# Kernel tuning notes

Hardware: AMD Instinct MI355X
Metric: run time of the kernel (lower is better)

## Reference

```python
import jax, jax.numpy as jnp
import numpy as np

N = 50000      # nodes
E = 800000     # edges (avg degree 16)
D_IN = 128
D_H = 128
D_OUT = 64


def setup_inputs() -> dict:
    key = jax.random.key(0)
    k_x, k_e, k_w1, k_b1, k_w2, k_b2 = jax.random.split(key, 6)
    x = jax.random.normal(k_x, (N, D_IN), dtype=jnp.float32)
    edge_index = jax.random.randint(k_e, (2, E), 0, N, dtype=jnp.int32)
    # Glorot-style init for GCN weights, zero bias (as in PyG GCNConv defaults)
    W1 = jax.random.normal(k_w1, (D_IN, D_H), dtype=jnp.float32) * (1.0 / np.sqrt(D_IN))
    b1 = jnp.zeros((D_H,), dtype=jnp.float32)
    W2 = jax.random.normal(k_w2, (D_H, D_OUT), dtype=jnp.float32) * (1.0 / np.sqrt(D_H))
    b2 = jnp.zeros((D_OUT,), dtype=jnp.float32)
    return {"x": x, "edge_index": edge_index, "W1": W1, "b1": b1, "W2": W2, "b2": b2}


def _gcn_norm(edge_index, n):
    # PyG gcn_norm with add_self_loops=True, edge_weight = 1
    loops = jnp.arange(n, dtype=edge_index.dtype)
    src = jnp.concatenate([edge_index[0], loops])  # [E+N]
    dst = jnp.concatenate([edge_index[1], loops])
    deg = jax.ops.segment_sum(jnp.ones_like(dst, dtype=jnp.float32), dst, num_segments=n)
    dinv = jnp.where(deg > 0, jax.lax.rsqrt(deg), 0.0)
    norm = dinv[src] * dinv[dst]                   # [E+N]
    return src, dst, norm


def _gcn_conv(h, src, dst, norm, W, b, n):
    # transform -> gather source -> scale by symmetric norm -> scatter-add at dst -> bias
    hW = h @ W                                      # [N, F_out]
    msg = hW[src] * norm[:, None]                   # [E+N, F_out]
    agg = jax.ops.segment_sum(msg, dst, num_segments=n)
    return agg + b


def reference(x, edge_index, W1, b1, W2, b2):
    n = x.shape[0]
    src, dst, norm = _gcn_norm(edge_index, n)
    x1 = jax.nn.relu(_gcn_conv(x, src, dst, norm, W1, b1, n))
    x2 = _gcn_conv(x1, src, dst, norm, W2, b2, n)
    return x2
```

## Files before the change

### kernel.cpp

```cpp
#include <hip/hip_runtime.h>

#define CAP  64
#define BN   64
#define NBMAX 1024
#define ECAP 2048
#define P1E  4096

typedef unsigned int uint;
typedef unsigned short ushort;
typedef __attribute__((ext_vector_type(8))) short short8;
typedef __attribute__((ext_vector_type(4))) float f32x4;

__device__ inline ushort f2bf(float f) {
    uint u = __float_as_uint(f);
    return (ushort)((u + 0x7fffu + ((u >> 16) & 1u)) >> 16);
}
__device__ inline uint packbf2(float lo, float hi) {
    return (uint)f2bf(lo) | ((uint)f2bf(hi) << 16);
}
__device__ inline void unpackbf2(uint u, float& lo, float& hi) {
    lo = __uint_as_float(u << 16);
    hi = __uint_as_float(u & 0xffff0000u);
}

__global__ __launch_bounds__(256) void k_init(const float* __restrict__ W1,
                                              const float* __restrict__ W2,
                                              ushort* __restrict__ W1t,
                                              ushort* __restrict__ W2t,
                                              int* __restrict__ gtail) {
    int i = blockIdx.x * 256 + threadIdx.x;
    if (i < NBMAX) gtail[i] = 0;
    if (i < 4 * 128 * 32) {
        int kt = i >> 12;
        int nn = (i >> 5) & 127;
        int ko = i & 31;
        W1t[i] = f2bf(W1[(size_t)(kt * 32 + ko) * 128 + nn]);
    }
    int j = i - 4 * 128 * 32;
    if (j >= 0 && j < 4 * 64 * 32) {
        int kt = j >> 11;
        int nn = (j >> 5) & 63;
        int ko = j & 31;
        W2t[j] = f2bf(W2[(size_t)(kt * 32 + ko) * 64 + nn]);
    }
}

__global__ __launch_bounds__(256) void k_part(const int* __restrict__ esrc,
                                              const int* __restrict__ edst,
                                              int E, int nb,
                                              int* __restrict__ gtail,
                                              uint* __restrict__ ebuf) {
    __shared__ int hist[NBMAX];
    int base_e = blockIdx.x * P1E;
    for (int i = threadIdx.x; i < nb; i += 256) hist[i] = 0;
    __syncthreads();

    int d[16], s[16];
#pragma unroll
    for (int u = 0; u < 16; u++) {
        int e = base_e + u * 256 + threadIdx.x;
        d[u] = (e < E) ? edst[e] : -1;
        s[u] = (e < E) ? esrc[e] : 0;
        if (d[u] >= 0) atomicAdd(&hist[d[u] >> 6], 1);
    }
    __syncthreads();

    for (int i = threadIdx.x; i < nb; i += 256) {
        int h = hist[i];
        hist[i] = (h > 0) ? atomicAdd(&gtail[i], h) : 0;
    }
    __syncthreads();

#pragma unroll
    for (int u = 0; u < 16; u++) {
        if (d[u] >= 0) {
            int b = d[u] >> 6;
            int slot = atomicAdd(&hist[b], 1);
            if (slot < ECAP)
                ebuf[(size_t)b * ECAP + slot] =
                    ((uint)(d[u] & (BN - 1)) << 16) | (uint)s[u];
        }
    }
}

__global__ __launch_bounds__(256) void k_csr(const uint* __restrict__ ebuf,
                                             const int* __restrict__ gtail,
                                             int n,
                                             ushort* __restrict__ colbuf,
                                             int* __restrict__ cnt,
                                             float* __restrict__ dinv) {
    __shared__ ushort cb[BN * CAP];
    __shared__ int cl[BN];
    int b = blockIdx.x;
    int ne = gtail[b];
    if (ne > ECAP) ne = ECAP;
    for (int i = threadIdx.x; i < BN; i += 256) cl[i] = 0;
    __syncthreads();

    const uint* eb = ebuf + (size_t)b * ECAP;
    for (int i = threadIdx.x; i < ne; i += 256) {
        uint pr = eb[i];
        int dloc = pr >> 16;
        int p = atomicAdd(&cl[dloc], 1);
        if (p < CAP) cb[dloc * CAP + p] = (ushort)(pr & 0xffffu);
    }
    __syncthreads();

    int node0 = b * BN;
    for (int i = threadIdx.x; i < BN * CAP / 8; i += 256) {
        int node = node0 + i / (CAP / 8);
        if (node < n)
            ((uint4*)&colbuf[(size_t)node0 * CAP])[i] = ((const uint4*)cb)[i];
    }
    for (int i = threadIdx.x; i < BN; i += 256) {
        int node = node0 + i;
        if (node < n) {
            int c = cl[i];
            dinv[node] = rsqrtf((float)c + 1.0f);
            cnt[node] = (c > CAP) ? CAP : c;
        }
    }
}

__global__ __launch_bounds__(256) void k_mgemm1(const float* __restrict__ Xf,
                                                const ushort* __restrict__ Wt,
                                                ushort* __restrict__ Yb, int n) {
    __shared__ ushort Ws[4 * 128 * 32];
    for (int idx = threadIdx.x; idx < 4 * 128 * 32 / 8; idx += 256)
        ((uint4*)Ws)[idx] = ((const uint4*)Wt)[idx];
    __syncthreads();

    int wid  = threadIdx.x >> 6;
    int l    = threadIdx.x & 63;
    int mrow = l & 15;
    int kgrp = l >> 4;
    int row16 = (blockIdx.x * 4 + wid) * 16;
    int r  = row16 + mrow;
    int rc = (r < n) ? r : (n - 1);

    f32x4 acc[8];
#pragma unroll
    for (int t = 0; t < 8; t++) acc[t] = (f32x4){0.f, 0.f, 0.f, 0.f};

#pragma unroll
    for (int kt = 0; kt < 4; kt++) {
        const float* xp = &Xf[(size_t)rc * 128 + kt * 32 + kgrp * 8];
        float4 x0 = *(const float4*)xp;
        float4 x1 = *(const float4*)(xp + 4);
        short8 a;
        a[0] = (short)f2bf(x0.x); a[1] = (short)f2bf(x0.y);
        a[2] = (short)f2bf(x0.z); a[3] = (short)f2bf(x0.w);
        a[4] = (short)f2bf(x1.x); a[5] = (short)f2bf(x1.y);
        a[6] = (short)f2bf(x1.z); a[7] = (short)f2bf(x1.w);
#pragma unroll
        for (int t = 0; t < 8; t++) {
            short8 b = *(const short8*)&Ws[((kt * 128) + t * 16 + mrow) * 32 + kgrp * 8];
            acc[t] = __builtin_amdgcn_mfma_f32_16x16x32_bf16(a, b, acc[t], 0, 0, 0);
        }
    }

    int orow = row16 + kgrp * 4;
#pragma unroll
    for (int t = 0; t < 8; t++) {
#pragma unroll
        for (int q = 0; q < 4; q++) {
            int rr = orow + q;
            if (rr < n) Yb[(size_t)rr * 128 + t * 16 + mrow] = f2bf(acc[t][q]);
        }
    }
}

__global__ __launch_bounds__(1024) void k_agg1m(const ushort* __restrict__ Hb,
                                                const int* __restrict__ cntc,
                                                const ushort* __restrict__ colbuf,
                                                const float* __restrict__ dinv,
                                                const float* __restrict__ b1,
                                                const ushort* __restrict__ W2t,
                                                ushort* __restrict__ Yb2, int n) {
    __shared__ ushort x1s[64 * 128];
    __shared__ ushort Ws[4 * 64 * 32];
    for (int idx = threadIdx.x; idx < 4 * 64 * 32 / 8; idx += 1024)
        ((uint4*)Ws)[idx] = ((const uint4*)W2t)[idx];

    const int CH = 128, LPG = 16;
    int grp  = threadIdx.x / LPG;
    int lane = threadIdx.x % LPG;
    int gid  = blockIdx.x * 64 + grp;
    int gc   = (gid < n) ? gid : (n - 1);

    float di = dinv[gc];
    int c = cntc[gc];
    if (c > CAP) c = CAP;

    float acc[8];
#pragma unroll
    for (int k = 0; k < 8; k++) acc[k] = 0.f;

    const ushort* cb = colbuf + (size_t)gc * CAP;
    for (int j = 0; j < c; j += 8) {
        uint4 iv = *(const uint4*)(cb + j);
        int s[8];
        s[0] = iv.x & 0xffff; s[1] = iv.x >> 16;
        s[2] = iv.y & 0xffff; s[3] = iv.y >> 16;
        s[4] = iv.z & 0xffff; s[5] = iv.z >> 16;
        s[6] = iv.w & 0xffff; s[7] = iv.w >> 16;
#pragma unroll
        for (int u = 1; u < 8; u++) if (j + u >= c) s[u] = s[0];
        float w[8];
#pragma unroll
        for (int u = 0; u < 8; u++)
            w[u] = (j + u < c) ? dinv[s[u]] : 0.f;
        uint4 h[8];
#pragma unroll
        for (int u = 0; u < 8; u++)
            h[u] = *(const uint4*)(Hb + (size_t)s[u] * CH + lane * 8);
#pragma unroll
        for (int u = 0; u < 8; u++) {
            float f0, f1;
            unpackbf2(h[u].x, f0, f1); acc[0] += f0 * w[u]; acc[1] += f1 * w[u];
            unpackbf2(h[u].y, f0, f1); acc[2] += f0 * w[u]; acc[3] += f1 * w[u];
            unpackbf2(h[u].z, f0, f1); acc[4] += f0 * w[u]; acc[5] += f1 * w[u];
            unpackbf2(h[u].w, f0, f1); acc[6] += f0 * w[u]; acc[7] += f1 * w[u];
        }
    }

    uint4 aself = *(const uint4*)(Hb + (size_t)gc * CH + lane * 8);
    float sf[8];
    unpackbf2(aself.x, sf[0], sf[1]);
    unpackbf2(aself.y, sf[2], sf[3]);
    unpackbf2(aself.z, sf[4], sf[5]);
    unpackbf2(aself.w, sf[6], sf[7]);

    float4 bb0 = *(const float4*)&b1[lane * 8];
    float4 bb1 = *(const float4*)&b1[lane * 8 + 4];
    float bb[8] = {bb0.x, bb0.y, bb0.z, bb0.w, bb1.x, bb1.y, bb1.z, bb1.w};

    float xv[8];
#pragma unroll
    for (int k = 0; k < 8; k++)
        xv[k] = fmaxf((acc[k] + di * sf[k]) * di + bb[k], 0.f);

    uint up[4] = { packbf2(xv[0], xv[1]), packbf2(xv[2], xv[3]),
                   packbf2(xv[4], xv[5]), packbf2(xv[6], xv[7]) };
    int slot = lane ^ (grp & 7);
    *(uint4*)&x1s[grp * 128 + slot * 8] = *(uint4*)up;

    __syncthreads();

    int wv = threadIdx.x >> 6;
    int l  = threadIdx.x & 63;
    int wr = wv >> 2, wc = wv & 3;
    int mrow = l & 15, kgrp = l >> 4;
    int arow = wr * 16 + mrow;

    f32x4 a2 = (f32x4){0.f, 0.f, 0.f, 0.f};
#pragma unroll
    for (int kt = 0; kt < 4; kt++) {
        int slotA = (kt * 4 + kgrp) ^ (arow & 7);
        short8 a = *(const short8*)&x1s[arow * 128 + slotA * 8];
        short8 b = *(const short8*)&Ws[((kt * 64) + wc * 16 + mrow) * 32 + kgrp * 8];
        a2 = __builtin_amdgcn_mfma_f32_16x16x32_bf16(a, b, a2, 0, 0, 0);
    }

    int row0 = blockIdx.x * 64 + wr * 16 + kgrp * 4;
#pragma unroll
    for (int q = 0; q < 4; q++) {
        int rr = row0 + q;
        if (rr < n) Yb2[(size_t)rr * 64 + wc * 16 + mrow] = f2bf(a2[q]);
    }
}

__global__ __launch_bounds__(256) void k_agg2(const ushort* __restrict__ Hb,
                                              const int* __restrict__ cntc,
                                              const ushort* __restrict__ colbuf,
                                              const float* __restrict__ dinv,
                                              const float* __restrict__ b2,
                                              float* __restrict__ out, int n) {
    const int CH = 64, LPG = 8;
    int t    = blockIdx.x * 256 + threadIdx.x;
    int gid  = t / LPG;
    int lane = t % LPG;
    if (gid >= n) return;

    float di = dinv[gid];
    int c = cntc[gid];
    if (c > CAP) c = CAP;

    float acc[8];
#pragma unroll
    for (int k = 0; k < 8; k++) acc[k] = 0.f;

    const ushort* cb = colbuf + (size_t)gid * CAP;
    for (int j = 0; j < c; j += 8) {
        uint4 iv = *(const uint4*)(cb + j);
        int s[8];
        s[0] = iv.x & 0xffff; s[1] = iv.x >> 16;
        s[2] = iv.y & 0xffff; s[3] = iv.y >> 16;
        s[4] = iv.z & 0xffff; s[5] = iv.z >> 16;
        s[6] = iv.w & 0xffff; s[7] = iv.w >> 16;
#pragma unroll
        for (int u = 1; u < 8; u++) if (j + u >= c) s[u] = s[0];
        float w[8];
#pragma unroll
        for (int u = 0; u < 8; u++)
            w[u] = (j + u < c) ? dinv[s[u]] : 0.f;
        uint4 h[8];
#pragma unroll
        for (int u = 0; u < 8; u++)
            h[u] = *(const uint4*)(Hb + (size_t)s[u] * CH + lane * 8);
#pragma unroll
        for (int u = 0; u < 8; u++) {
            float f0, f1;
            unpackbf2(h[u].x, f0, f1); acc[0] += f0 * w[u]; acc[1] += f1 * w[u];
            unpackbf2(h[u].y, f0, f1); acc[2] += f0 * w[u]; acc[3] += f1 * w[u];
            unpackbf2(h[u].z, f0, f1); acc[4] += f0 * w[u]; acc[5] += f1 * w[u];
            unpackbf2(h[u].w, f0, f1); acc[6] += f0 * w[u]; acc[7] += f1 * w[u];
        }
    }

    uint4 aself = *(const uint4*)(Hb + (size_t)gid * CH + lane * 8);
    float sf[8];
    unpackbf2(aself.x, sf[0], sf[1]);
    unpackbf2(aself.y, sf[2], sf[3]);
    unpackbf2(aself.z, sf[4], sf[5]);
    unpackbf2(aself.w, sf[6], sf[7]);

    float4 bb0 = *(const float4*)&b2[lane * 8];
    float4 bb1 = *(const float4*)&b2[lane * 8 + 4];
    float bb[8] = {bb0.x, bb0.y, bb0.z, bb0.w, bb1.x, bb1.y, bb1.z, bb1.w};

    float o[8];
#pragma unroll
    for (int k = 0; k < 8; k++)
        o[k] = (acc[k] + di * sf[k]) * di + bb[k];

    float* dst = out + (size_t)gid * CH + lane * 8;
    *(float4*)dst       = make_float4(o[0], o[1], o[2], o[3]);
    *(float4*)(dst + 4) = make_float4(o[4], o[5], o[6], o[7]);
}

extern "C" void kernel_launch(void* const* d_in, const int* in_sizes, int n_in,
                              void* d_out, int out_size, void* d_ws, size_t ws_size,
                              hipStream_t stream) {
    const float* x  = (const float*)d_in[0];
    const int*   ei = (const int*)d_in[1];
    const float* W1 = (const float*)d_in[2];
    const float* b1 = (const float*)d_in[3];
    const float* W2 = (const float*)d_in[4];
    const float* b2 = (const float*)d_in[5];
    float* out = (float*)d_out;

    int N = in_sizes[0] / 128;
    int E = in_sizes[1] / 2;
    const int* esrc = ei;
    const int* edst = ei + E;

    int nb = (N + BN - 1) / BN;

    char* ws = (char*)d_ws;
    size_t off = 0;
    auto alloc = [&](size_t bytes) -> void* {
        off = (off + 255) & ~(size_t)255;
        void* p = ws + off;
        off += bytes;
        return p;
    };
    int*    gtail   = (int*)   alloc((size_t)NBMAX * 4);
    int*    cnt     = (int*)   alloc((size_t)N * 4);
    float*  dinv    = (float*) alloc((size_t)N * 4);
    uint*   ebuf    = (uint*)  alloc((size_t)nb * ECAP * 4);
    ushort* colbuf  = (ushort*)alloc((size_t)nb * BN * CAP * 2 + 256);
    ushort* hW1b    = (ushort*)alloc((size_t)N * 128 * 2);
    ushort* hW2b    = (ushort*)alloc((size_t)N * 64 * 2);
    ushort* W1t     = (ushort*)alloc((size_t)4 * 128 * 32 * 2);
    ushort* W2t     = (ushort*)alloc((size_t)4 * 64 * 32 * 2);

    k_init<<<96, 256, 0, stream>>>(W1, W2, W1t, W2t, gtail);

    int nbP1 = (E + P1E - 1) / P1E;
    k_part<<<nbP1, 256, 0, stream>>>(esrc, edst, E, nb, gtail, ebuf);
    k_mgemm1<<<(N + 63) / 64, 256, 0, stream>>>(x, W1t, hW1b, N);
    k_csr<<<nb, 256, 0, stream>>>(ebuf, gtail, N, colbuf, cnt, dinv);

    k_agg1m<<<nb, 1024, 0, stream>>>(hW1b, cnt, colbuf, dinv, b1, W2t, hW2b, N);

    k_agg2<<<((size_t)N * 8 + 255) / 256, 256, 0, stream>>>(
        hW2b, cnt, colbuf, dinv, b2, out, N);
}
```

Measured before the change: 98.08 us.

## Split fused layer-1 aggregation and second GEMM into separate kernels

The fused 1024-thread aggregation+GEMM kernel is split into a 256-thread aggregation kernel that writes the layer-1 activations to a new bf16 buffer, plus a standalone MFMA GEMM kernel for the second layer. This removes the block-wide barrier and large shared-memory footprint so more blocks can be resident. Both aggregation kernels also gather 16 neighbors per iteration instead of 8 and hoist the self-row and bias loads ahead of the loop to expose more memory parallelism. The cost is an extra launch and a round-trip of the N×128 bf16 activations through global memory, plus higher register pressure from the wider unroll.

```diff
diff --git a/kernel.cpp b/kernel.cpp
--- a/kernel.cpp
+++ b/kernel.cpp
@@ -170,52 +170,94 @@
     }
 }
 
-__global__ __launch_bounds__(1024) void k_agg1m(const ushort* __restrict__ Hb,
-                                                const int* __restrict__ cntc,
-                                                const ushort* __restrict__ colbuf,
-                                                const float* __restrict__ dinv,
-                                                const float* __restrict__ b1,
-                                                const ushort* __restrict__ W2t,
-                                                ushort* __restrict__ Yb2, int n) {
-    __shared__ ushort x1s[64 * 128];
+__global__ __launch_bounds__(256) void k_mgemm2(const ushort* __restrict__ Xh,
+                                                const ushort* __restrict__ Wt,
+                                                ushort* __restrict__ Yb, int n) {
     __shared__ ushort Ws[4 * 64 * 32];
-    for (int idx = threadIdx.x; idx < 4 * 64 * 32 / 8; idx += 1024)
-        ((uint4*)Ws)[idx] = ((const uint4*)W2t)[idx];
-
+    for (int idx = threadIdx.x; idx < 4 * 64 * 32 / 8; idx += 256)
+        ((uint4*)Ws)[idx] = ((const uint4*)Wt)[idx];
+    __syncthreads();
+
+    int wid  = threadIdx.x >> 6;
+    int l    = threadIdx.x & 63;
+    int mrow = l & 15;
+    int kgrp = l >> 4;
+    int row16 = (blockIdx.x * 4 + wid) * 16;
+    int r  = row16 + mrow;
+    int rc = (r < n) ? r : (n - 1);
+
+    f32x4 acc[4];
+#pragma unroll
+    for (int t = 0; t < 4; t++) acc[t] = (f32x4){0.f, 0.f, 0.f, 0.f};
+
+#pragma unroll
+    for (int kt = 0; kt < 4; kt++) {
+        short8 a = *(const short8*)&Xh[(size_t)rc * 128 + kt * 32 + kgrp * 8];
+#pragma unroll
+        for (int t = 0; t < 4; t++) {
+            short8 b = *(const short8*)&Ws[((kt * 64) + t * 16 + mrow) * 32 + kgrp * 8];
+            acc[t] = __builtin_amdgcn_mfma_f32_16x16x32_bf16(a, b, acc[t], 0, 0, 0);
+        }
+    }
+
+    int orow = row16 + kgrp * 4;
+#pragma unroll
+    for (int t = 0; t < 4; t++) {
+#pragma unroll
+        for (int q = 0; q < 4; q++) {
+            int rr = orow + q;
+            if (rr < n) Yb[(size_t)rr * 64 + t * 16 + mrow] = f2bf(acc[t][q]);
+        }
+    }
+}
+
+__global__ __launch_bounds__(256) void k_agg1(const ushort* __restrict__ Hb,
+                                              const int* __restrict__ cntc,
+                                              const ushort* __restrict__ colbuf,
+                                              const float* __restrict__ dinv,
+                                              const float* __restrict__ b1,
+                                              ushort* __restrict__ x1b, int n) {
     const int CH = 128, LPG = 16;
-    int grp  = threadIdx.x / LPG;
-    int lane = threadIdx.x % LPG;
-    int gid  = blockIdx.x * 64 + grp;
-    int gc   = (gid < n) ? gid : (n - 1);
-
-    float di = dinv[gc];
-    int c = cntc[gc];
+    int t    = blockIdx.x * 256 + threadIdx.x;
+    int gid  = t / LPG;
+    int lane = t % LPG;
+    if (gid >= n) return;
+
+    float di = dinv[gid];
+    int c = cntc[gid];
     if (c > CAP) c = CAP;
 
+    uint4 aself = *(const uint4*)(Hb + (size_t)gid * CH + lane * 8);
+    float4 bb0 = *(const float4*)&b1[lane * 8];
+    float4 bb1 = *(const float4*)&b1[lane * 8 + 4];
+
     float acc[8];
 #pragma unroll
     for (int k = 0; k < 8; k++) acc[k] = 0.f;
 
-    const ushort* cb = colbuf + (size_t)gc * CAP;
-    for (int j = 0; j < c; j += 8) {
-        uint4 iv = *(const uint4*)(cb + j);
-        int s[8];
-        s[0] = iv.x & 0xffff; s[1] = iv.x >> 16;
-        s[2] = iv.y & 0xffff; s[3] = iv.y >> 16;
-        s[4] = iv.z & 0xffff; s[5] = iv.z >> 16;
-        s[6] = iv.w & 0xffff; s[7] = iv.w >> 16;
-#pragma unroll
-        for (int u = 1; u < 8; u++) if (j + u >= c) s[u] = s[0];
-        float w[8];
-#pragma unroll
-        for (int u = 0; u < 8; u++)
+    const ushort* cb = colbuf + (size_t)gid * CAP;
+    for (int j = 0; j < c; j += 16) {
+        uint4 iv0 = *(const uint4*)(cb + j);
+        uint4 iv1 = *(const uint4*)(cb + j + 8);
+        uint ivw[8] = {iv0.x, iv0.y, iv0.z, iv0.w, iv1.x, iv1.y, iv1.z, iv1.w};
+        int s[16];
+#pragma unroll
+        for (int u = 0; u < 8; u++) {
+            s[2 * u]     = ivw[u] & 0xffff;
+            s[2 * u + 1] = ivw[u] >> 16;
+        }
+#pragma unroll
+        for (int u = 1; u < 16; u++) if (j + u >= c) s[u] = s[0];
+        float w[16];
+#pragma unroll
+        for (int u = 0; u < 16; u++)
             w[u] = (j + u < c) ? dinv[s[u]] : 0.f;
-        uint4 h[8];
-#pragma unroll
-        for (int u = 0; u < 8; u++)
+        uint4 h[16];
+#pragma unroll
+        for (int u = 0; u < 16; u++)
             h[u] = *(const uint4*)(Hb + (size_t)s[u] * CH + lane * 8);
 #pragma unroll
-        for (int u = 0; u < 8; u++) {
+        for (int u = 0; u < 16; u++) {
             float f0, f1;
             unpackbf2(h[u].x, f0, f1); acc[0] += f0 * w[u]; acc[1] += f1 * w[u];
             unpackbf2(h[u].y, f0, f1); acc[2] += f0 * w[u]; acc[3] += f1 * w[u];
@@ -224,15 +266,11 @@
         }
     }
 
-    uint4 aself = *(const uint4*)(Hb + (size_t)gc * CH + lane * 8);
     float sf[8];
     unpackbf2(aself.x, sf[0], sf[1]);
     unpackbf2(aself.y, sf[2], sf[3]);
     unpackbf2(aself.z, sf[4], sf[5]);
     unpackbf2(aself.w, sf[6], sf[7]);
-
-    float4 bb0 = *(const float4*)&b1[lane * 8];
-    float4 bb1 = *(const float4*)&b1[lane * 8 + 4];
     float bb[8] = {bb0.x, bb0.y, bb0.z, bb0.w, bb1.x, bb1.y, bb1.z, bb1.w};
 
     float xv[8];
@@ -242,32 +280,7 @@
 
     uint up[4] = { packbf2(xv[0], xv[1]), packbf2(xv[2], xv[3]),
                    packbf2(xv[4], xv[5]), packbf2(xv[6], xv[7]) };
-    int slot = lane ^ (grp & 7);
-    *(uint4*)&x1s[grp * 128 + slot * 8] = *(uint4*)up;
-
-    __syncthreads();
-
-    int wv = threadIdx.x >> 6;
-    int l  = threadIdx.x & 63;
-    int wr = wv >> 2, wc = wv & 3;
-    int mrow = l & 15, kgrp = l >> 4;
-    int arow = wr * 16 + mrow;
-
-    f32x4 a2 = (f32x4){0.f, 0.f, 0.f, 0.f};
-#pragma unroll
-    for (int kt = 0; kt < 4; kt++) {
-        int slotA = (kt * 4 + kgrp) ^ (arow & 7);
-        short8 a = *(const short8*)&x1s[arow * 128 + slotA * 8];
-        short8 b = *(const short8*)&Ws[((kt * 64) + wc * 16 + mrow) * 32 + kgrp * 8];
-        a2 = __builtin_amdgcn_mfma_f32_16x16x32_bf16(a, b, a2, 0, 0, 0);
-    }
-
-    int row0 = blockIdx.x * 64 + wr * 16 + kgrp * 4;
-#pragma unroll
-    for (int q = 0; q < 4; q++) {
-        int rr = row0 + q;
-        if (rr < n) Yb2[(size_t)rr * 64 + wc * 16 + mrow] = f2bf(a2[q]);
-    }
+    *(uint4*)&x1b[(size_t)gid * CH + lane * 8] = *(uint4*)up;
 }
 
 __global__ __launch_bounds__(256) void k_agg2(const ushort* __restrict__ Hb,
@@ -286,30 +299,37 @@
     int c = cntc[gid];
     if (c > CAP) c = CAP;
 
+    uint4 aself = *(const uint4*)(Hb + (size_t)gid * CH + lane * 8);
+    float4 bb0 = *(const float4*)&b2[lane * 8];
+    float4 bb1 = *(const float4*)&b2[lane * 8 + 4];
+
     float acc[8];
 #pragma unroll
     for (int k = 0; k < 8; k++) acc[k] = 0.f;
 
     const ushort* cb = colbuf + (size_t)gid * CAP;
-    for (int j = 0; j < c; j += 8) {
-        uint4 iv = *(const uint4*)(cb + j);
-        int s[8];
-        s[0] = iv.x & 0xffff; s[1] = iv.x >> 16;
-        s[2] = iv.y & 0xffff; s[3] = iv.y >> 16;
-        s[4] = iv.z & 0xffff; s[5] = iv.z >> 16;
-        s[6] = iv.w & 0xffff; s[7] = iv.w >> 16;
-#pragma unroll
-        for (int u = 1; u < 8; u++) if (j + u >= c) s[u] = s[0];
-        float w[8];
-#pragma unroll
-        for (int u = 0; u < 8; u++)
+    for (int j = 0; j < c; j += 16) {
+        uint4 iv0 = *(const uint4*)(cb + j);
+        uint4 iv1 = *(const uint4*)(cb + j + 8);
+        uint ivw[8] = {iv0.x, iv0.y, iv0.z, iv0.w, iv1.x, iv1.y, iv1.z, iv1.w};
+        int s[16];
+#pragma unroll
+        for (int u = 0; u < 8; u++) {
+            s[2 * u]     = ivw[u] & 0xffff;
+            s[2 * u + 1] = ivw[u] >> 16;
+        }
+#pragma unroll
+        for (int u = 1; u < 16; u++) if (j + u >= c) s[u] = s[0];
+        float w[16];
+#pragma unroll
+        for (int u = 0; u < 16; u++)
             w[u] = (j + u < c) ? dinv[s[u]] : 0.f;
-        uint4 h[8];
-#pragma unroll
-        for (int u = 0; u < 8; u++)
+        uint4 h[16];
+#pragma unroll
+        for (int u = 0; u < 16; u++)
             h[u] = *(const uint4*)(Hb + (size_t)s[u] * CH + lane * 8);
 #pragma unroll
-        for (int u = 0; u < 8; u++) {
+        for (int u = 0; u < 16; u++) {
             float f0, f1;
             unpackbf2(h[u].x, f0, f1); acc[0] += f0 * w[u]; acc[1] += f1 * w[u];
             unpackbf2(h[u].y, f0, f1); acc[2] += f0 * w[u]; acc[3] += f1 * w[u];
@@ -318,15 +338,11 @@
         }
     }
 
-    uint4 aself = *(const uint4*)(Hb + (size_t)gid * CH + lane * 8);
     float sf[8];
     unpackbf2(aself.x, sf[0], sf[1]);
     unpackbf2(aself.y, sf[2], sf[3]);
     unpackbf2(aself.z, sf[4], sf[5]);
     unpackbf2(aself.w, sf[6], sf[7]);
-
-    float4 bb0 = *(const float4*)&b2[lane * 8];
-    float4 bb1 = *(const float4*)&b2[lane * 8 + 4];
     float bb[8] = {bb0.x, bb0.y, bb0.z, bb0.w, bb1.x, bb1.y, bb1.z, bb1.w};
 
     float o[8];
@@ -371,6 +387,7 @@
     uint*   ebuf    = (uint*)  alloc((size_t)nb * ECAP * 4);
     ushort* colbuf  = (ushort*)alloc((size_t)nb * BN * CAP * 2 + 256);
     ushort* hW1b    = (ushort*)alloc((size_t)N * 128 * 2);
+    ushort* x1b     = (ushort*)alloc((size_t)N * 128 * 2);
     ushort* hW2b    = (ushort*)alloc((size_t)N * 64 * 2);
     ushort* W1t     = (ushort*)alloc((size_t)4 * 128 * 32 * 2);
     ushort* W2t     = (ushort*)alloc((size_t)4 * 64 * 32 * 2);
@@ -382,7 +399,10 @@
     k_mgemm1<<<(N + 63) / 64, 256, 0, stream>>>(x, W1t, hW1b, N);
     k_csr<<<nb, 256, 0, stream>>>(ebuf, gtail, N, colbuf, cnt, dinv);
 
-    k_agg1m<<<nb, 1024, 0, stream>>>(hW1b, cnt, colbuf, dinv, b1, W2t, hW2b, N);
+    k_agg1<<<((size_t)N * 16 + 255) / 256, 256, 0, stream>>>(
+        hW1b, cnt, colbuf, dinv, b1, x1b, N);
+
+    k_mgemm2<<<(N + 63) / 64, 256, 0, stream>>>(x1b, W2t, hW2b, N);
 
     k_agg2<<<((size_t)N * 8 + 255) / 256, 256, 0, stream>>>(
         hW2b, cnt, colbuf, dinv, b2, out, N);
```

Result: faster. 93.86 us (-4.3%).
